# Kernel tuning notes

Hardware: AMD Instinct MI355X
Metric: run time of the kernel (lower is better)

The kernel has to match this reference:

```python
import jax, jax.numpy as jnp
import numpy as np

N = 50000      # nodes
E = 800000     # edges (before self-loops)
F_IN = 256     # num_features
H = 8          # heads (conv1)
C = 32         # hidden_size per head (conv1)
OUT = 2        # conv2 out channels (1 head)
NEG_SLOPE = 0.2


def setup_inputs() -> dict:
    key = jax.random.key(0)
    ks = jax.random.split(key, 12)
    x = jax.random.normal(ks[0], (N, F_IN), jnp.float32)
    edge_index = jax.random.randint(ks[1], (2, E), 0, N, dtype=jnp.int64)

    def glorot(k, shape):
        fan = shape[0] if len(shape) == 2 else int(np.prod(shape))
        s = float(np.sqrt(6.0 / (fan + shape[-1])))
        return jax.random.uniform(k, shape, jnp.float32, -s, s)

    W1 = glorot(ks[2], (F_IN, H * C))
    att_src1 = glorot(ks[3], (H, C))
    att_dst1 = glorot(ks[4], (H, C))
    b1 = jnp.zeros((H * C,), jnp.float32)
    W2 = glorot(ks[5], (H * C, 1 * OUT))
    att_src2 = glorot(ks[6], (1, OUT))
    att_dst2 = glorot(ks[7], (1, OUT))
    b2 = jnp.zeros((OUT,), jnp.float32)
    return {"x": x, "edge_index": edge_index, "W1": W1, "att_src1": att_src1,
            "att_dst1": att_dst1, "b1": b1, "W2": W2, "att_src2": att_src2,
            "att_dst2": att_dst2, "b2": b2}


def gat_conv(x, src, dst, W, a_src, a_dst, b, heads, ch, n):
    # x: [n, f] -> projected [n, heads, ch]
    xp = (x @ W).reshape(n, heads, ch)
    alpha_src = jnp.einsum('nhc,hc->nh', xp, a_src)   # [n, H]
    alpha_dst = jnp.einsum('nhc,hc->nh', xp, a_dst)   # [n, H]
    e = jax.nn.leaky_relu(alpha_src[src] + alpha_dst[dst], NEG_SLOPE)  # [E', H]
    # segment softmax over edges grouped by destination node
    m = jax.ops.segment_max(e, dst, num_segments=n)                    # [n, H]
    p = jnp.exp(e - m[dst])
    denom = jax.ops.segment_sum(p, dst, num_segments=n)                # [n, H]
    alpha = p / denom[dst]                                             # [E', H]
    # weighted scatter-aggregate of source messages
    out = jax.ops.segment_sum(xp[src] * alpha[:, :, None], dst, num_segments=n)
    return out.reshape(n, heads * ch) + b


def reference(x, edge_index, W1, att_src1, att_dst1, b1, W2, att_src2, att_dst2, b2):
    n = x.shape[0]
    loops = jnp.arange(n, dtype=edge_index.dtype)  # GATConv add_self_loops=True
    src = jnp.concatenate([edge_index[0], loops])
    dst = jnp.concatenate([edge_index[1], loops])
    h = jax.nn.relu(gat_conv(x, src, dst, W1, att_src1, att_dst1, b1, H, C, n))
    # eval mode: F.dropout and attention dropout are identity
    return gat_conv(h, src, dst, W2, att_src2, att_dst2, b2, 1, OUT, n)
```

## Files before the change

kernel.cpp:

```cpp
#include <hip/hip_runtime.h>
#include <math.h>

#define N_NODES 50000
#define N_EDGES 800000
#define EP (N_EDGES + N_NODES)
#define NEG 0.2f
#define SCAN_BLOCKS 49

typedef __attribute__((ext_vector_type(8))) short bf16x8;
typedef __attribute__((ext_vector_type(4))) float f32x4;
typedef __attribute__((ext_vector_type(2))) float f32x2;

static __device__ __forceinline__ unsigned short bf16_rn(float f) {
    union { float f; unsigned int u; } v; v.f = f;
    unsigned int u = v.u;
    unsigned int r = (u + 0x7FFFu + ((u >> 16) & 1u)) >> 16;
    return (unsigned short)r;
}
static __device__ __forceinline__ float bf16_tof(unsigned short u) {
    union { unsigned int u; float f; } v; v.u = ((unsigned int)u) << 16;
    return v.f;
}
static __device__ __forceinline__ f32x2 bf2_unpack(unsigned int u) {
    union { unsigned int i; float f; } a, b;
    a.i = u << 16; b.i = u & 0xFFFF0000u;
    return (f32x2){a.f, b.f};
}


__global__ void k_hist(const int* __restrict__ ei, int* __restrict__ counts) {
    int e = blockIdx.x * 256 + threadIdx.x;
    if (e >= EP) return;
    int d = (e < N_EDGES) ? ei[N_EDGES + e] : (e - N_EDGES);
    atomicAdd(&counts[d], 1);
}

__global__ void k_scan_block(const int* __restrict__ counts, int* __restrict__ excl,
                             int* __restrict__ bsums) {
    __shared__ int wsum[4];
    int b = blockIdx.x, t = threadIdx.x;
    int lane = t & 63, w = t >> 6;
    int i0 = b * 1024 + t * 4;
    int v0 = (i0 + 0 < N_NODES) ? counts[i0 + 0] : 0;
    int v1 = (i0 + 1 < N_NODES) ? counts[i0 + 1] : 0;
    int v2 = (i0 + 2 < N_NODES) ? counts[i0 + 2] : 0;
    int v3 = (i0 + 3 < N_NODES) ? counts[i0 + 3] : 0;
    int s = v0 + v1 + v2 + v3;
    int incl = s;
    #pragma unroll
    for (int d = 1; d < 64; d <<= 1) {
        int u = __shfl_up(incl, d);
        if (lane >= d) incl += u;
    }
    if (lane == 63) wsum[w] = incl;
    __syncthreads();
    if (t == 0) {
        int run = 0;
        #pragma unroll
        for (int i = 0; i < 4; ++i) { int x = wsum[i]; wsum[i] = run; run += x; }
        bsums[b] = run;
    }
    __syncthreads();
    int base = wsum[w] + incl - s;
    if (i0 + 0 < N_NODES) excl[i0 + 0] = base;
    if (i0 + 1 < N_NODES) excl[i0 + 1] = base + v0;
    if (i0 + 2 < N_NODES) excl[i0 + 2] = base + v0 + v1;
    if (i0 + 3 < N_NODES) excl[i0 + 3] = base + v0 + v1 + v2;
}

__global__ void k_scan_add(int* __restrict__ row_ptr, const int* __restrict__ bsums) {
    __shared__ int soff;
    int b = blockIdx.x, t = threadIdx.x;
    if (t < 64) {
        int v = (t < SCAN_BLOCKS) ? bsums[t] : 0;
        int incl = v;
        #pragma unroll
        for (int d = 1; d < 64; d <<= 1) {
            int u = __shfl_up(incl, d);
            if (t >= d) incl += u;
        }
        if (t == b) soff = incl - v;
    }
    __syncthreads();
    int off = soff;
    int i0 = b * 1024 + t * 4;
    #pragma unroll
    for (int j = 0; j < 4; ++j)
        if (i0 + j < N_NODES) row_ptr[i0 + j] += off;
    if (b == 0 && t == 0) row_ptr[N_NODES] = EP;
}

__global__ void k_scatter(const int* __restrict__ ei, const int* __restrict__ row_ptr,
                          int* __restrict__ fill, int* __restrict__ colb) {
    int e = blockIdx.x * 256 + threadIdx.x;
    if (e >= EP) return;
    int s, d;
    if (e < N_EDGES) { s = ei[e]; d = ei[N_EDGES + e]; }
    else             { s = e - N_EDGES; d = s; }
    int pos = row_ptr[d] + atomicAdd(&fill[d], 1);
    colb[pos] = s;
}

__global__ void k_cvtWfrag(const float* __restrict__ W1, bf16x8* __restrict__ Wfrag) {
    int ft = blockIdx.x * 256 + threadIdx.x;
    int c = ft >> 10, rem = ft & 1023;
    int nt = rem >> 6, l = rem & 63;
    int n = (l & 15) * 16 + nt;
    int k0 = c * 32 + (l >> 4) * 8;
    bf16x8 f;
    #pragma unroll
    for (int j = 0; j < 8; ++j)
        f[j] = (short)bf16_rn(W1[(k0 + j) * 256 + n]);
    Wfrag[ft] = f;
}

#define GM_GRID 782
__global__ __launch_bounds__(128) void
k_gemm1m(const float* __restrict__ x, const bf16x8* __restrict__ Wfrag,
         unsigned short* __restrict__ xp1b,
         const float* __restrict__ asrc, const float* __restrict__ adst,
         float* __restrict__ as1, float* __restrict__ ad1) {
    __shared__ bf16x8 lds[1024];
    int t = threadIdx.x, l = t & 63, w = t >> 6;
    int rowbase = blockIdx.x * 64 + w * 32;
    int m = l & 15, kg = l >> 4;

    f32x4 acc0[16], acc1[16];
    #pragma unroll
    for (int nt = 0; nt < 16; ++nt) {
        acc0[nt] = (f32x4){0.f, 0.f, 0.f, 0.f};
        acc1[nt] = (f32x4){0.f, 0.f, 0.f, 0.f};
    }

    int r0 = rowbase + m;
    int r1 = rowbase + 16 + m;
    if (r0 > N_NODES - 1) r0 = N_NODES - 1;
    if (r1 > N_NODES - 1) r1 = N_NODES - 1;
    const float4* x4 = (const float4*)x;

    for (int c = 0; c < 8; ++c) {
        __syncthreads();
        const bf16x8* src = Wfrag + c * 1024;
        #pragma unroll
        for (int q = 0; q < 8; ++q)
            lds[q * 128 + t] = src[q * 128 + t];
        __syncthreads();

        int kb = (c * 32 + kg * 8) >> 2;
        float4 xa0 = x4[r0 * 64 + kb], xb0 = x4[r0 * 64 + kb + 1];
        float4 xa1 = x4[r1 * 64 + kb], xb1 = x4[r1 * 64 + kb + 1];
        bf16x8 aF0, aF1;
        aF0[0] = (short)bf16_rn(xa0.x); aF0[1] = (short)bf16_rn(xa0.y);
        aF0[2] = (short)bf16_rn(xa0.z); aF0[3] = (short)bf16_rn(xa0.w);
        aF0[4] = (short)bf16_rn(xb0.x); aF0[5] = (short)bf16_rn(xb0.y);
        aF0[6] = (short)bf16_rn(xb0.z); aF0[7] = (short)bf16_rn(xb0.w);
        aF1[0] = (short)bf16_rn(xa1.x); aF1[1] = (short)bf16_rn(xa1.y);
        aF1[2] = (short)bf16_rn(xa1.z); aF1[3] = (short)bf16_rn(xa1.w);
        aF1[4] = (short)bf16_rn(xb1.x); aF1[5] = (short)bf16_rn(xb1.y);
        aF1[6] = (short)bf16_rn(xb1.z); aF1[7] = (short)bf16_rn(xb1.w);

        #pragma unroll
        for (int nt = 0; nt < 16; ++nt) {
            bf16x8 bF = lds[nt * 64 + l];
            acc0[nt] = __builtin_amdgcn_mfma_f32_16x16x32_bf16(aF0, bF, acc0[nt], 0, 0, 0);
            acc1[nt] = __builtin_amdgcn_mfma_f32_16x16x32_bf16(aF1, bF, acc1[nt], 0, 0, 0);
        }
    }

    int cbase = l & 15, rq = l >> 4;
    float asV[16], adV[16];
    #pragma unroll
    for (int q = 0; q < 4; ++q) {
        float4 sa = ((const float4*)asrc)[cbase * 4 + q];
        float4 da = ((const float4*)adst)[cbase * 4 + q];
        asV[q * 4 + 0] = sa.x; asV[q * 4 + 1] = sa.y; asV[q * 4 + 2] = sa.z; asV[q * 4 + 3] = sa.w;
        adV[q * 4 + 0] = da.x; adV[q * 4 + 1] = da.y; adV[q * 4 + 2] = da.z; adV[q * 4 + 3] = da.w;
    }
    #pragma unroll
    for (int g = 0; g < 2; ++g) {
        f32x4* A = g ? acc1 : acc0;
        #pragma unroll
        for (int reg = 0; reg < 4; ++reg) {
            int gr = rowbase + g * 16 + rq * 4 + reg;
            unsigned int ob[8];
            float ps = 0.f, pd = 0.f;
            #pragma unroll
            for (int q = 0; q < 8; ++q) {
                float v0 = A[2 * q][reg], v1 = A[2 * q + 1][reg];
                ob[q] = (unsigned int)bf16_rn(v0) | ((unsigned int)bf16_rn(v1) << 16);
                ps = fmaf(v0, asV[2 * q], ps);     ps = fmaf(v1, asV[2 * q + 1], ps);
                pd = fmaf(v0, adV[2 * q], pd);     pd = fmaf(v1, adV[2 * q + 1], pd);
            }
            ps += __shfl_xor(ps, 1);
            pd += __shfl_xor(pd, 1);
            if (gr < N_NODES) {
                uint4* dst = (uint4*)(xp1b + gr * 256 + cbase * 16);
                dst[0] = make_uint4(ob[0], ob[1], ob[2], ob[3]);
                dst[1] = make_uint4(ob[4], ob[5], ob[6], ob[7]);
                if ((l & 1) == 0) {
                    as1[gr * 8 + (cbase >> 1)] = ps;
                    ad1[gr * 8 + (cbase >> 1)] = pd;
                }
            }
        }
    }
}

__global__ void k_agg1(const ushort4* __restrict__ xpb, const float* __restrict__ as1,
                       const float* __restrict__ ad1, const int* __restrict__ row_ptr,
                       const int* __restrict__ colb, const float* __restrict__ b1,
                       const float* __restrict__ W2, const float* __restrict__ as2w,
                       const float* __restrict__ ad2w,
                       float* __restrict__ xp2, float* __restrict__ as2,
                       float* __restrict__ ad2) {
    int t = threadIdx.x, l = t & 63, w = t >> 6;
    int n = blockIdx.x * 4 + w;
    int hidx = l >> 3;
    float adn = ad1[n * 8 + hidx];
    int start = row_ptr[n], end = row_ptr[n + 1];
    const uint2* xp2v = (const uint2*)xpb;
    f32x2 accA = {0.f, 0.f}, accB = {0.f, 0.f};
    float den = 0.f;
    int j = start;
    for (; j + 4 <= end; j += 4) {
        int s0 = colb[j], s1 = colb[j + 1], s2 = colb[j + 2], s3 = colb[j + 3];
        uint2 r0 = xp2v[s0 * 64 + l];
        uint2 r1 = xp2v[s1 * 64 + l];
        uint2 r2 = xp2v[s2 * 64 + l];
        uint2 r3 = xp2v[s3 * 64 + l];
        float e0 = as1[s0 * 8 + hidx] + adn;
        float e1 = as1[s1 * 8 + hidx] + adn;
        float e2 = as1[s2 * 8 + hidx] + adn;
        float e3 = as1[s3 * 8 + hidx] + adn;
        e0 = (e0 > 0.f) ? e0 : NEG * e0;
        e1 = (e1 > 0.f) ? e1 : NEG * e1;
        e2 = (e2 > 0.f) ? e2 : NEG * e2;
        e3 = (e3 > 0.f) ? e3 : NEG * e3;
        float p0 = __expf(e0), p1 = __expf(e1), p2 = __expf(e2), p3 = __expf(e3);
        den += (p0 + p1) + (p2 + p3);
        f32x2 q0 = {p0, p0}, q1 = {p1, p1}, q2 = {p2, p2}, q3 = {p3, p3};
        accA += q0 * bf2_unpack(r0.x);  accB += q0 * bf2_unpack(r0.y);
        accA += q1 * bf2_unpack(r1.x);  accB += q1 * bf2_unpack(r1.y);
        accA += q2 * bf2_unpack(r2.x);  accB += q2 * bf2_unpack(r2.y);
        accA += q3 * bf2_unpack(r3.x);  accB += q3 * bf2_unpack(r3.y);
    }
    for (; j < end; ++j) {
        int s = colb[j];
        uint2 r = xp2v[s * 64 + l];
        float e = as1[s * 8 + hidx] + adn;
        e = (e > 0.f) ? e : NEG * e;
        float p = __expf(e);
        den += p;
        f32x2 q = {p, p};
        accA += q * bf2_unpack(r.x);
        accB += q * bf2_unpack(r.y);
    }
    float4 bv = ((const float4*)b1)[l];
    float inv = 1.f / den;
    float4 o;
    o.x = fmaxf(accA[0] * inv + bv.x, 0.f);
    o.y = fmaxf(accA[1] * inv + bv.y, 0.f);
    o.z = fmaxf(accB[0] * inv + bv.z, 0.f);
    o.w = fmaxf(accB[1] * inv + bv.w, 0.f);
    float4 wa = ((const float4*)W2)[2 * l];
    float4 wb = ((const float4*)W2)[2 * l + 1];
    float d0 = o.x * wa.x + o.y * wa.z + o.z * wb.x + o.w * wb.z;
    float d1 = o.x * wa.y + o.y * wa.w + o.z * wb.y + o.w * wb.w;
    #pragma unroll
    for (int m = 1; m < 64; m <<= 1) {
        d0 += __shfl_xor(d0, m);
        d1 += __shfl_xor(d1, m);
    }
    if (l == 0) {
        xp2[2 * n] = d0;
        xp2[2 * n + 1] = d1;
        as2[n] = d0 * as2w[0] + d1 * as2w[1];
        ad2[n] = d0 * ad2w[0] + d1 * ad2w[1];
    }
}

__global__ void k_agg2(const float* __restrict__ xp2, const float* __restrict__ as2,
                       const float* __restrict__ ad2, const int* __restrict__ row_ptr,
                       const int* __restrict__ colb, const float* __restrict__ b2,
                       float* __restrict__ out) {
    int t = threadIdx.x, l = t & 63, w = t >> 6;
    int n = blockIdx.x * 4 + w;
    int start = row_ptr[n], end = row_ptr[n + 1];
    float adn = ad2[n];
    float a0 = 0.f, a1 = 0.f, den = 0.f;
    for (int j = start + l; j < end; j += 64) {
        int s = colb[j];
        float e = as2[s] + adn;
        e = (e > 0.f) ? e : NEG * e;
        float p = __expf(e);
        den += p;
        a0 = fmaf(p, xp2[2 * s], a0);
        a1 = fmaf(p, xp2[2 * s + 1], a1);
    }
    #pragma unroll
    for (int m = 1; m < 64; m <<= 1) {
        a0 += __shfl_xor(a0, m);
        a1 += __shfl_xor(a1, m);
        den += __shfl_xor(den, m);
    }
    if (l == 0) {
        out[2 * n] = a0 / den + b2[0];
        out[2 * n + 1] = a1 / den + b2[1];
    }
}

extern "C" void kernel_launch(void* const* d_in, const int* in_sizes, int n_in,
                              void* d_out, int out_size, void* d_ws, size_t ws_size,
                              hipStream_t stream) {
    const float* x     = (const float*)d_in[0];
    const int*   ei    = (const int*)d_in[1];
    const float* W1    = (const float*)d_in[2];
    const float* asrc1 = (const float*)d_in[3];
    const float* adst1 = (const float*)d_in[4];
    const float* b1    = (const float*)d_in[5];
    const float* W2    = (const float*)d_in[6];
    const float* asrc2 = (const float*)d_in[7];
    const float* adst2 = (const float*)d_in[8];
    const float* b2    = (const float*)d_in[9];
    float* out = (float*)d_out;

    char* ws = (char*)d_ws;
    unsigned short* xp1b = (unsigned short*)(ws + 0);
    bf16x8* Wfrag  = (bf16x8*)(ws + 25600000);
    float* as1     = (float*)(ws + 102400000);
    float* ad1     = (float*)(ws + 104000000);
    float* xp2     = (float*)(ws + 105600000);
    float* as2     = (float*)(ws + 106000000);
    float* ad2     = (float*)(ws + 106200000);
    int*   counts  = (int*)  (ws + 106400000);
    int*   fill    = (int*)  (ws + 106600000);
    int*   row_ptr = (int*)  (ws + 106800000);
    int*   colb    = (int*)  (ws + 107000064);
    int*   bsums   = (int*)  (ws + 110400064);

    hipMemsetAsync(counts, 0, 400000, stream);

    int egrid = (EP + 255) / 256;
    k_hist      <<<egrid,       256, 0, stream>>>(ei, counts);
    k_scan_block<<<SCAN_BLOCKS, 256, 0, stream>>>(counts, row_ptr, bsums);
    k_scan_add  <<<SCAN_BLOCKS, 256, 0, stream>>>(row_ptr, bsums);
    k_scatter   <<<egrid,       256, 0, stream>>>(ei, row_ptr, fill, colb);

    k_cvtWfrag  <<<32,     256, 0, stream>>>(W1, Wfrag);
    k_gemm1m    <<<GM_GRID, 128, 0, stream>>>(x, Wfrag, xp1b, asrc1, adst1, as1, ad1);
    k_agg1      <<<12500,  256, 0, stream>>>((const ushort4*)xp1b, as1, ad1, row_ptr, colb,
                                             b1, W2, asrc2, adst2, xp2, as2, ad2);
    k_agg2      <<<12500,  256, 0, stream>>>(xp2, as2, ad2, row_ptr, colb, b2, out);
}
```

Measured before the change: 290.6 us.

## Fuse CSR build into cooperative kernel, interleave attention scores, retune aggregation

Merges the memset, histogram, two scan passes, scatter and weight conversion into one cooperative kernel that uses grid-wide syncs, removing several launches. The source attention score is now stored inline after each bf16 feature row (640-byte stride), so one gather per neighbor brings both values. k_agg1 unrolls by 8 and broadcasts neighbor indices with readfirstlane. k_agg2 switches from a wavefront per node to a thread per node. Risks include grid-sync overhead, a larger footprint for the padded rows, and load imbalance on high-degree nodes in layer 2.

Measured after the change: 421.3 us. +45.0%, slower.

```diff
diff --git a/kernel.cpp b/kernel.cpp
--- a/kernel.cpp
+++ b/kernel.cpp
@@ -1,11 +1,17 @@
 #include <hip/hip_runtime.h>
+#include <hip/hip_cooperative_groups.h>
 #include <math.h>
+
+namespace cg = cooperative_groups;
 
 #define N_NODES 50000
 #define N_EDGES 800000
 #define EP (N_EDGES + N_NODES)
 #define NEG 0.2f
 #define SCAN_BLOCKS 49
+#define BLD_BLOCKS 256
+#define BLD_THREADS 65536
+#define ROW_US 320
 
 typedef __attribute__((ext_vector_type(8))) short bf16x8;
 typedef __attribute__((ext_vector_type(4))) float f32x4;
@@ -17,101 +23,102 @@
     unsigned int r = (u + 0x7FFFu + ((u >> 16) & 1u)) >> 16;
     return (unsigned short)r;
 }
-static __device__ __forceinline__ float bf16_tof(unsigned short u) {
-    union { unsigned int u; float f; } v; v.u = ((unsigned int)u) << 16;
-    return v.f;
-}
 static __device__ __forceinline__ f32x2 bf2_unpack(unsigned int u) {
     union { unsigned int i; float f; } a, b;
     a.i = u << 16; b.i = u & 0xFFFF0000u;
     return (f32x2){a.f, b.f};
 }
 
-
-__global__ void k_hist(const int* __restrict__ ei, int* __restrict__ counts) {
-    int e = blockIdx.x * 256 + threadIdx.x;
-    if (e >= EP) return;
-    int d = (e < N_EDGES) ? ei[N_EDGES + e] : (e - N_EDGES);
-    atomicAdd(&counts[d], 1);
-}
-
-__global__ void k_scan_block(const int* __restrict__ counts, int* __restrict__ excl,
-                             int* __restrict__ bsums) {
+__global__ void k_build(const int* __restrict__ ei, int* __restrict__ counts,
+                        int* __restrict__ fill, int* __restrict__ row_ptr,
+                        int* __restrict__ bsums, int* __restrict__ colb,
+                        const float* __restrict__ W1, bf16x8* __restrict__ Wfrag) {
+    cg::grid_group grid = cg::this_grid();
     __shared__ int wsum[4];
-    int b = blockIdx.x, t = threadIdx.x;
-    int lane = t & 63, w = t >> 6;
-    int i0 = b * 1024 + t * 4;
-    int v0 = (i0 + 0 < N_NODES) ? counts[i0 + 0] : 0;
-    int v1 = (i0 + 1 < N_NODES) ? counts[i0 + 1] : 0;
-    int v2 = (i0 + 2 < N_NODES) ? counts[i0 + 2] : 0;
-    int v3 = (i0 + 3 < N_NODES) ? counts[i0 + 3] : 0;
-    int s = v0 + v1 + v2 + v3;
-    int incl = s;
-    #pragma unroll
-    for (int d = 1; d < 64; d <<= 1) {
-        int u = __shfl_up(incl, d);
-        if (lane >= d) incl += u;
-    }
-    if (lane == 63) wsum[w] = incl;
-    __syncthreads();
-    if (t == 0) {
-        int run = 0;
-        #pragma unroll
-        for (int i = 0; i < 4; ++i) { int x = wsum[i]; wsum[i] = run; run += x; }
-        bsums[b] = run;
-    }
-    __syncthreads();
-    int base = wsum[w] + incl - s;
-    if (i0 + 0 < N_NODES) excl[i0 + 0] = base;
-    if (i0 + 1 < N_NODES) excl[i0 + 1] = base + v0;
-    if (i0 + 2 < N_NODES) excl[i0 + 2] = base + v0 + v1;
-    if (i0 + 3 < N_NODES) excl[i0 + 3] = base + v0 + v1 + v2;
-}
-
-__global__ void k_scan_add(int* __restrict__ row_ptr, const int* __restrict__ bsums) {
     __shared__ int soff;
-    int b = blockIdx.x, t = threadIdx.x;
-    if (t < 64) {
-        int v = (t < SCAN_BLOCKS) ? bsums[t] : 0;
-        int incl = v;
+    int t = threadIdx.x, b = blockIdx.x;
+    int tid = b * 256 + t;
+
+    for (int i = tid; i < 2 * N_NODES; i += BLD_THREADS) counts[i] = 0;
+    if (tid < 8192) {
+        int ft = tid;
+        int c = ft >> 10, rem = ft & 1023;
+        int nt = rem >> 6, l = rem & 63;
+        int n = (l & 15) * 16 + nt;
+        int k0 = c * 32 + (l >> 4) * 8;
+        bf16x8 f;
+        #pragma unroll
+        for (int j = 0; j < 8; ++j)
+            f[j] = (short)bf16_rn(W1[(k0 + j) * 256 + n]);
+        Wfrag[ft] = f;
+    }
+    grid.sync();
+
+    for (int e = tid; e < EP; e += BLD_THREADS) {
+        int d = (e < N_EDGES) ? ei[N_EDGES + e] : (e - N_EDGES);
+        atomicAdd(&counts[d], 1);
+    }
+    grid.sync();
+
+    if (b < SCAN_BLOCKS) {
+        int lane = t & 63, w = t >> 6;
+        int i0 = b * 1024 + t * 4;
+        int v0 = (i0 + 0 < N_NODES) ? counts[i0 + 0] : 0;
+        int v1 = (i0 + 1 < N_NODES) ? counts[i0 + 1] : 0;
+        int v2 = (i0 + 2 < N_NODES) ? counts[i0 + 2] : 0;
+        int v3 = (i0 + 3 < N_NODES) ? counts[i0 + 3] : 0;
+        int s = v0 + v1 + v2 + v3;
+        int incl = s;
         #pragma unroll
         for (int d = 1; d < 64; d <<= 1) {
             int u = __shfl_up(incl, d);
-            if (t >= d) incl += u;
-        }
-        if (t == b) soff = incl - v;
-    }
-    __syncthreads();
-    int off = soff;
-    int i0 = b * 1024 + t * 4;
-    #pragma unroll
-    for (int j = 0; j < 4; ++j)
-        if (i0 + j < N_NODES) row_ptr[i0 + j] += off;
-    if (b == 0 && t == 0) row_ptr[N_NODES] = EP;
-}
-
-__global__ void k_scatter(const int* __restrict__ ei, const int* __restrict__ row_ptr,
-                          int* __restrict__ fill, int* __restrict__ colb) {
-    int e = blockIdx.x * 256 + threadIdx.x;
-    if (e >= EP) return;
-    int s, d;
-    if (e < N_EDGES) { s = ei[e]; d = ei[N_EDGES + e]; }
-    else             { s = e - N_EDGES; d = s; }
-    int pos = row_ptr[d] + atomicAdd(&fill[d], 1);
-    colb[pos] = s;
-}
-
-__global__ void k_cvtWfrag(const float* __restrict__ W1, bf16x8* __restrict__ Wfrag) {
-    int ft = blockIdx.x * 256 + threadIdx.x;
-    int c = ft >> 10, rem = ft & 1023;
-    int nt = rem >> 6, l = rem & 63;
-    int n = (l & 15) * 16 + nt;
-    int k0 = c * 32 + (l >> 4) * 8;
-    bf16x8 f;
-    #pragma unroll
-    for (int j = 0; j < 8; ++j)
-        f[j] = (short)bf16_rn(W1[(k0 + j) * 256 + n]);
-    Wfrag[ft] = f;
+            if (lane >= d) incl += u;
+        }
+        if (lane == 63) wsum[w] = incl;
+        __syncthreads();
+        if (t == 0) {
+            int run = 0;
+            #pragma unroll
+            for (int i = 0; i < 4; ++i) { int x = wsum[i]; wsum[i] = run; run += x; }
+            bsums[b] = run;
+        }
+        __syncthreads();
+        int base = wsum[w] + incl - s;
+        if (i0 + 0 < N_NODES) row_ptr[i0 + 0] = base;
+        if (i0 + 1 < N_NODES) row_ptr[i0 + 1] = base + v0;
+        if (i0 + 2 < N_NODES) row_ptr[i0 + 2] = base + v0 + v1;
+        if (i0 + 3 < N_NODES) row_ptr[i0 + 3] = base + v0 + v1 + v2;
+    }
+    grid.sync();
+
+    if (b < SCAN_BLOCKS) {
+        if (t < 64) {
+            int v = (t < SCAN_BLOCKS) ? bsums[t] : 0;
+            int incl = v;
+            #pragma unroll
+            for (int d = 1; d < 64; d <<= 1) {
+                int u = __shfl_up(incl, d);
+                if (t >= d) incl += u;
+            }
+            if (t == b) soff = incl - v;
+        }
+        __syncthreads();
+        int off = soff;
+        int i0 = b * 1024 + t * 4;
+        #pragma unroll
+        for (int j = 0; j < 4; ++j)
+            if (i0 + j < N_NODES) row_ptr[i0 + j] += off;
+        if (b == 0 && t == 0) row_ptr[N_NODES] = EP;
+    }
+    grid.sync();
+
+    for (int e = tid; e < EP; e += BLD_THREADS) {
+        int s, d;
+        if (e < N_EDGES) { s = ei[e]; d = ei[N_EDGES + e]; }
+        else             { s = e - N_EDGES; d = s; }
+        int pos = row_ptr[d] + atomicAdd(&fill[d], 1);
+        colb[pos] = s;
+    }
 }
 
 #define GM_GRID 782
@@ -119,7 +126,7 @@
 k_gemm1m(const float* __restrict__ x, const bf16x8* __restrict__ Wfrag,
          unsigned short* __restrict__ xp1b,
          const float* __restrict__ asrc, const float* __restrict__ adst,
-         float* __restrict__ as1, float* __restrict__ ad1) {
+         float* __restrict__ ad1) {
     __shared__ bf16x8 lds[1024];
     int t = threadIdx.x, l = t & 63, w = t >> 6;
     int rowbase = blockIdx.x * 64 + w * 32;
@@ -194,11 +201,12 @@
             ps += __shfl_xor(ps, 1);
             pd += __shfl_xor(pd, 1);
             if (gr < N_NODES) {
-                uint4* dst = (uint4*)(xp1b + gr * 256 + cbase * 16);
+                unsigned short* row = xp1b + (size_t)gr * ROW_US;
+                uint4* dst = (uint4*)(row + cbase * 16);
                 dst[0] = make_uint4(ob[0], ob[1], ob[2], ob[3]);
                 dst[1] = make_uint4(ob[4], ob[5], ob[6], ob[7]);
                 if ((l & 1) == 0) {
-                    as1[gr * 8 + (cbase >> 1)] = ps;
+                    ((float*)(row + 256))[cbase >> 1] = ps;
                     ad1[gr * 8 + (cbase >> 1)] = pd;
                 }
             }
@@ -206,11 +214,10 @@
     }
 }
 
-__global__ void k_agg1(const ushort4* __restrict__ xpb, const float* __restrict__ as1,
-                       const float* __restrict__ ad1, const int* __restrict__ row_ptr,
-                       const int* __restrict__ colb, const float* __restrict__ b1,
-                       const float* __restrict__ W2, const float* __restrict__ as2w,
-                       const float* __restrict__ ad2w,
+__global__ void k_agg1(const unsigned short* __restrict__ xp1b, const float* __restrict__ ad1,
+                       const int* __restrict__ row_ptr, const int* __restrict__ colb,
+                       const float* __restrict__ b1, const float* __restrict__ W2,
+                       const float* __restrict__ as2w, const float* __restrict__ ad2w,
                        float* __restrict__ xp2, float* __restrict__ as2,
                        float* __restrict__ ad2) {
     int t = threadIdx.x, l = t & 63, w = t >> 6;
@@ -218,40 +225,75 @@
     int hidx = l >> 3;
     float adn = ad1[n * 8 + hidx];
     int start = row_ptr[n], end = row_ptr[n + 1];
-    const uint2* xp2v = (const uint2*)xpb;
+    const char* xb = (const char*)xp1b;
+    int loff = 8 * l;
+    int aoff = 512 + 4 * hidx;
     f32x2 accA = {0.f, 0.f}, accB = {0.f, 0.f};
     float den = 0.f;
     int j = start;
-    for (; j + 4 <= end; j += 4) {
-        int s0 = colb[j], s1 = colb[j + 1], s2 = colb[j + 2], s3 = colb[j + 3];
-        uint2 r0 = xp2v[s0 * 64 + l];
-        uint2 r1 = xp2v[s1 * 64 + l];
-        uint2 r2 = xp2v[s2 * 64 + l];
-        uint2 r3 = xp2v[s3 * 64 + l];
-        float e0 = as1[s0 * 8 + hidx] + adn;
-        float e1 = as1[s1 * 8 + hidx] + adn;
-        float e2 = as1[s2 * 8 + hidx] + adn;
-        float e3 = as1[s3 * 8 + hidx] + adn;
+    for (; j + 8 <= end; j += 8) {
+        int s0 = __builtin_amdgcn_readfirstlane(colb[j]);
+        int s1 = __builtin_amdgcn_readfirstlane(colb[j + 1]);
+        int s2 = __builtin_amdgcn_readfirstlane(colb[j + 2]);
+        int s3 = __builtin_amdgcn_readfirstlane(colb[j + 3]);
+        int s4 = __builtin_amdgcn_readfirstlane(colb[j + 4]);
+        int s5 = __builtin_amdgcn_readfirstlane(colb[j + 5]);
+        int s6 = __builtin_amdgcn_readfirstlane(colb[j + 6]);
+        int s7 = __builtin_amdgcn_readfirstlane(colb[j + 7]);
+        const char* p0 = xb + (size_t)s0 * 640;
+        const char* p1 = xb + (size_t)s1 * 640;
+        const char* p2 = xb + (size_t)s2 * 640;
+        const char* p3 = xb + (size_t)s3 * 640;
+        const char* p4 = xb + (size_t)s4 * 640;
+        const char* p5 = xb + (size_t)s5 * 640;
+        const char* p6 = xb + (size_t)s6 * 640;
+        const char* p7 = xb + (size_t)s7 * 640;
+        uint2 r0 = *(const uint2*)(p0 + loff);
+        uint2 r1 = *(const uint2*)(p1 + loff);
+        uint2 r2 = *(const uint2*)(p2 + loff);
+        uint2 r3 = *(const uint2*)(p3 + loff);
+        uint2 r4 = *(const uint2*)(p4 + loff);
+        uint2 r5 = *(const uint2*)(p5 + loff);
+        uint2 r6 = *(const uint2*)(p6 + loff);
+        uint2 r7 = *(const uint2*)(p7 + loff);
+        float e0 = *(const float*)(p0 + aoff) + adn;
+        float e1 = *(const float*)(p1 + aoff) + adn;
+        float e2 = *(const float*)(p2 + aoff) + adn;
+        float e3 = *(const float*)(p3 + aoff) + adn;
+        float e4 = *(const float*)(p4 + aoff) + adn;
+        float e5 = *(const float*)(p5 + aoff) + adn;
+        float e6 = *(const float*)(p6 + aoff) + adn;
+        float e7 = *(const float*)(p7 + aoff) + adn;
         e0 = (e0 > 0.f) ? e0 : NEG * e0;
         e1 = (e1 > 0.f) ? e1 : NEG * e1;
         e2 = (e2 > 0.f) ? e2 : NEG * e2;
         e3 = (e3 > 0.f) ? e3 : NEG * e3;
-        float p0 = __expf(e0), p1 = __expf(e1), p2 = __expf(e2), p3 = __expf(e3);
-        den += (p0 + p1) + (p2 + p3);
-        f32x2 q0 = {p0, p0}, q1 = {p1, p1}, q2 = {p2, p2}, q3 = {p3, p3};
-        accA += q0 * bf2_unpack(r0.x);  accB += q0 * bf2_unpack(r0.y);
-        accA += q1 * bf2_unpack(r1.x);  accB += q1 * bf2_unpack(r1.y);
-        accA += q2 * bf2_unpack(r2.x);  accB += q2 * bf2_unpack(r2.y);
-        accA += q3 * bf2_unpack(r3.x);  accB += q3 * bf2_unpack(r3.y);
+        e4 = (e4 > 0.f) ? e4 : NEG * e4;
+        e5 = (e5 > 0.f) ? e5 : NEG * e5;
+        e6 = (e6 > 0.f) ? e6 : NEG * e6;
+        e7 = (e7 > 0.f) ? e7 : NEG * e7;
+        float p0e = __expf(e0), p1e = __expf(e1), p2e = __expf(e2), p3e = __expf(e3);
+        float p4e = __expf(e4), p5e = __expf(e5), p6e = __expf(e6), p7e = __expf(e7);
+        den += ((p0e + p1e) + (p2e + p3e)) + ((p4e + p5e) + (p6e + p7e));
+        f32x2 q;
+        q = (f32x2){p0e, p0e}; accA += q * bf2_unpack(r0.x); accB += q * bf2_unpack(r0.y);
+        q = (f32x2){p1e, p1e}; accA += q * bf2_unpack(r1.x); accB += q * bf2_unpack(r1.y);
+        q = (f32x2){p2e, p2e}; accA += q * bf2_unpack(r2.x); accB += q * bf2_unpack(r2.y);
+        q = (f32x2){p3e, p3e}; accA += q * bf2_unpack(r3.x); accB += q * bf2_unpack(r3.y);
+        q = (f32x2){p4e, p4e}; accA += q * bf2_unpack(r4.x); accB += q * bf2_unpack(r4.y);
+        q = (f32x2){p5e, p5e}; accA += q * bf2_unpack(r5.x); accB += q * bf2_unpack(r5.y);
+        q = (f32x2){p6e, p6e}; accA += q * bf2_unpack(r6.x); accB += q * bf2_unpack(r6.y);
+        q = (f32x2){p7e, p7e}; accA += q * bf2_unpack(r7.x); accB += q * bf2_unpack(r7.y);
     }
     for (; j < end; ++j) {
-        int s = colb[j];
-        uint2 r = xp2v[s * 64 + l];
-        float e = as1[s * 8 + hidx] + adn;
+        int s = __builtin_amdgcn_readfirstlane(colb[j]);
+        const char* p = xb + (size_t)s * 640;
+        uint2 r = *(const uint2*)(p + loff);
+        float e = *(const float*)(p + aoff) + adn;
         e = (e > 0.f) ? e : NEG * e;
-        float p = __expf(e);
-        den += p;
-        f32x2 q = {p, p};
+        float pe = __expf(e);
+        den += pe;
+        f32x2 q = {pe, pe};
         accA += q * bf2_unpack(r.x);
         accB += q * bf2_unpack(r.y);
     }
@@ -283,30 +325,25 @@
                        const float* __restrict__ ad2, const int* __restrict__ row_ptr,
                        const int* __restrict__ colb, const float* __restrict__ b2,
                        float* __restrict__ out) {
-    int t = threadIdx.x, l = t & 63, w = t >> 6;
-    int n = blockIdx.x * 4 + w;
+    int n = blockIdx.x * 256 + threadIdx.x;
+    if (n >= N_NODES) return;
     int start = row_ptr[n], end = row_ptr[n + 1];
     float adn = ad2[n];
+    float b20 = b2[0], b21 = b2[1];
     float a0 = 0.f, a1 = 0.f, den = 0.f;
-    for (int j = start + l; j < end; j += 64) {
+    const float2* xpv = (const float2*)xp2;
+    for (int j = start; j < end; ++j) {
         int s = colb[j];
         float e = as2[s] + adn;
         e = (e > 0.f) ? e : NEG * e;
         float p = __expf(e);
         den += p;
-        a0 = fmaf(p, xp2[2 * s], a0);
-        a1 = fmaf(p, xp2[2 * s + 1], a1);
-    }
-    #pragma unroll
-    for (int m = 1; m < 64; m <<= 1) {
-        a0 += __shfl_xor(a0, m);
-        a1 += __shfl_xor(a1, m);
-        den += __shfl_xor(den, m);
-    }
-    if (l == 0) {
-        out[2 * n] = a0 / den + b2[0];
-        out[2 * n + 1] = a1 / den + b2[1];
-    }
+        float2 v = xpv[s];
+        a0 = fmaf(p, v.x, a0);
+        a1 = fmaf(p, v.y, a1);
+    }
+    float inv = 1.f / den;
+    ((float2*)out)[n] = make_float2(a0 * inv + b20, a1 * inv + b21);
 }
 
 extern "C" void kernel_launch(void* const* d_in, const int* in_sizes, int n_in,
@@ -326,29 +363,24 @@
 
     char* ws = (char*)d_ws;
     unsigned short* xp1b = (unsigned short*)(ws + 0);
-    bf16x8* Wfrag  = (bf16x8*)(ws + 25600000);
-    float* as1     = (float*)(ws + 102400000);
-    float* ad1     = (float*)(ws + 104000000);
-    float* xp2     = (float*)(ws + 105600000);
-    float* as2     = (float*)(ws + 106000000);
-    float* ad2     = (float*)(ws + 106200000);
-    int*   counts  = (int*)  (ws + 106400000);
-    int*   fill    = (int*)  (ws + 106600000);
-    int*   row_ptr = (int*)  (ws + 106800000);
-    int*   colb    = (int*)  (ws + 107000064);
-    int*   bsums   = (int*)  (ws + 110400064);
-
-    hipMemsetAsync(counts, 0, 400000, stream);
-
-    int egrid = (EP + 255) / 256;
-    k_hist      <<<egrid,       256, 0, stream>>>(ei, counts);
-    k_scan_block<<<SCAN_BLOCKS, 256, 0, stream>>>(counts, row_ptr, bsums);
-    k_scan_add  <<<SCAN_BLOCKS, 256, 0, stream>>>(row_ptr, bsums);
-    k_scatter   <<<egrid,       256, 0, stream>>>(ei, row_ptr, fill, colb);
-
-    k_cvtWfrag  <<<32,     256, 0, stream>>>(W1, Wfrag);
-    k_gemm1m    <<<GM_GRID, 128, 0, stream>>>(x, Wfrag, xp1b, asrc1, adst1, as1, ad1);
-    k_agg1      <<<12500,  256, 0, stream>>>((const ushort4*)xp1b, as1, ad1, row_ptr, colb,
-                                             b1, W2, asrc2, adst2, xp2, as2, ad2);
-    k_agg2      <<<12500,  256, 0, stream>>>(xp2, as2, ad2, row_ptr, colb, b2, out);
-}
+    bf16x8* Wfrag  = (bf16x8*)(ws + 32000000);
+    float* ad1     = (float*)(ws + 32200000);
+    float* xp2     = (float*)(ws + 33800000);
+    float* as2     = (float*)(ws + 34200000);
+    float* ad2     = (float*)(ws + 34400000);
+    int*   counts  = (int*)  (ws + 34600000);
+    int*   fill    = (int*)  (ws + 34800000);
+    int*   row_ptr = (int*)  (ws + 35000000);
+    int*   colb    = (int*)  (ws + 35200064);
+    int*   bsums   = (int*)  (ws + 38600064);
+
+    void* bargs[] = {(void*)&ei, (void*)&counts, (void*)&fill, (void*)&row_ptr,
+                     (void*)&bsums, (void*)&colb, (void*)&W1, (void*)&Wfrag};
+    hipLaunchCooperativeKernel((void*)k_build, dim3(BLD_BLOCKS), dim3(256),
+                               bargs, 0, stream);
+
+    k_gemm1m <<<GM_GRID, 128, 0, stream>>>(x, Wfrag, xp1b, asrc1, adst1, ad1);
+    k_agg1   <<<12500,  256, 0, stream>>>(xp1b, ad1, row_ptr, colb,
+                                          b1, W2, asrc2, adst2, xp2, as2, ad2);
+    k_agg2   <<<196,    256, 0, stream>>>(xp2, as2, ad2, row_ptr, colb, b2, out);
+}
```
